# Kernel tuning notes

Measured on AMD Instinct MI355X. Metric: run time of the kernel, lower is better.

## Reference

```python
import jax, jax.numpy as jnp
import numpy as np

D_MODEL = 1024
NUM_HEADS = 16
D_HEAD = D_MODEL // NUM_HEADS
D_FF = 4096
B, T = 2, 2048
THETA = 10000.0
EPS = 1e-5


def setup_inputs() -> dict:
    key = jax.random.key(0)
    ks = jax.random.split(key, 6)
    def tn(k, shape, fan_in, fan_out):
        std = np.sqrt(2.0 / (fan_in + fan_out))
        return jax.random.normal(k, shape, dtype=jnp.float32) * std
    return {
        "x": jax.random.normal(ks[0], (B, T, D_MODEL), dtype=jnp.float32),
        "W_qkv": tn(ks[1], (3 * D_MODEL, D_MODEL), D_MODEL, 3 * D_MODEL),
        "W_o": tn(ks[2], (D_MODEL, D_MODEL), D_MODEL, D_MODEL),
        "g1": jnp.ones((D_MODEL,), dtype=jnp.float32),
        "g2": jnp.ones((D_MODEL,), dtype=jnp.float32),
        "W1": tn(ks[3], (D_FF, D_MODEL), D_MODEL, D_FF),
        "W2": tn(ks[4], (D_MODEL, D_FF), D_FF, D_MODEL),
        "W3": tn(ks[5], (D_FF, D_MODEL), D_MODEL, D_FF),
    }


def _rmsnorm(x, g):
    xf = x.astype(jnp.float32)
    rms = jnp.sqrt(jnp.mean(xf * xf, axis=-1, keepdims=True) + EPS)
    return (xf / rms * g).astype(x.dtype)


def _rope(t, cos, sin):
    # t: [B,H,T,dh]; interleaved (even,odd) pairs treated as complex numbers
    tr = t.reshape(*t.shape[:-1], D_HEAD // 2, 2)
    te, to = tr[..., 0], tr[..., 1]
    out = jnp.stack([te * cos - to * sin, te * sin + to * cos], axis=-1)
    return out.reshape(t.shape)


def reference(x, W_qkv, W_o, g1, g2, W1, W2, W3):
    Bx, Tx, C = x.shape
    # --- attention sub-block (pre-norm) ---
    h = _rmsnorm(x, g1)
    qkv = jnp.einsum('btc,jc->btj', h, W_qkv)                # [B,T,3C]
    qkv = qkv.reshape(Bx, Tx, 3, NUM_HEADS, D_HEAD)
    qkv = jnp.transpose(qkv, (2, 0, 3, 1, 4))                # [3,B,H,T,dh]
    q, k, v = qkv[0], qkv[1], qkv[2]
    # RoPE tables for positions arange(T)
    inv = 1.0 / (THETA ** (jnp.arange(0, D_HEAD, 2, dtype=jnp.float32) / D_HEAD))
    ang = jnp.arange(Tx, dtype=jnp.float32)[:, None] * inv[None, :]   # [T,dh/2]
    cos, sin = jnp.cos(ang), jnp.sin(ang)                    # broadcast over B,H
    q = _rope(q, cos, sin)
    k = _rope(k, cos, sin)
    scores = jnp.einsum('bhqd,bhkd->bhqk', q, k) / jnp.sqrt(jnp.float32(D_HEAD))
    causal = jnp.tril(jnp.ones((Tx, Tx), dtype=bool))
    scores = jnp.where(causal, scores, -jnp.inf)
    probs = jax.nn.softmax(scores, axis=-1)
    attn = jnp.einsum('bhqk,bhkd->bhqd', probs, v)           # [B,H,T,dh]
    attn = jnp.transpose(attn, (0, 2, 1, 3)).reshape(Bx, Tx, C)
    x = x + jnp.einsum('btc,jc->btj', attn, W_o)
    # --- SwiGLU FFN sub-block (pre-norm) ---
    h2 = _rmsnorm(x, g2)
    a = jnp.einsum('btc,fc->btf', h2, W1)
    b = jnp.einsum('btc,fc->btf', h2, W3)
    ffn = jnp.einsum('btf,cf->btc', (a * jax.nn.sigmoid(a)) * b, W2)
    return x + ffn
```

## Files before the change

### kernel.cpp

```cpp
#include <hip/hip_runtime.h>
#include <math.h>

typedef __bf16 bf16_t;
typedef __bf16 bf16x2 __attribute__((ext_vector_type(2)));
typedef __bf16 bf16x4 __attribute__((ext_vector_type(4)));
typedef __bf16 bf16x8 __attribute__((ext_vector_type(8)));
typedef float  f32x4  __attribute__((ext_vector_type(4)));

#define D_MODEL 1024
#define T_SEQ   2048
#define BATCH   2
#define NHEAD   16
#define DHEAD   64
#define DFF     4096
#define ROWS    (BATCH * T_SEQ)

static __device__ __forceinline__ void gload_lds16(const void* g, void* l) {
  __builtin_amdgcn_global_load_lds((const __attribute__((address_space(1))) void*)g,
                                   (__attribute__((address_space(3))) void*)l,
                                   16, 0, 0);
}

__global__ __launch_bounds__(256) void cvt_all_kernel(const float* __restrict__ Wqkv,
                                                      const float* __restrict__ Wo,
                                                      const float* __restrict__ W1,
                                                      const float* __restrict__ W3,
                                                      const float* __restrict__ W2,
                                                      bf16_t* __restrict__ wq,
                                                      bf16_t* __restrict__ wo,
                                                      bf16_t* __restrict__ w13,
                                                      bf16_t* __restrict__ w2) {
  int i = blockIdx.x * 256 + threadIdx.x;
  const float* src; bf16_t* dst; int off;
  if (i < 786432)       { src = Wqkv; dst = wq;            off = i; }
  else if (i < 1048576) { src = Wo;   dst = wo;            off = i - 786432; }
  else if (i < 2097152) { src = W1;   dst = w13;           off = i - 1048576; }
  else if (i < 3145728) { src = W3;   dst = w13 + 4194304; off = i - 2097152; }
  else                  { src = W2;   dst = w2;            off = i - 3145728; }
  float4 v = ((const float4*)src)[off];
  bf16x4 o;
  o[0] = (bf16_t)v.x; o[1] = (bf16_t)v.y; o[2] = (bf16_t)v.z; o[3] = (bf16_t)v.w;
  *(bf16x4*)(dst + off * 4) = o;
}

__global__ __launch_bounds__(256) void rope_tables_kernel(float* __restrict__ cost,
                                                          float* __restrict__ sint) {
  int i = blockIdx.x * 256 + threadIdx.x;
  int t = i >> 5, p = i & 31;
  double inv = pow(10000.0, -(double)(2 * p) / 64.0);
  double ang = (double)t * inv;
  cost[i] = (float)cos(ang);
  sint[i] = (float)sin(ang);
}

__global__ __launch_bounds__(256) void rmsnorm_kernel(const float* __restrict__ x,
                                                      const float* __restrict__ g,
                                                      bf16_t* __restrict__ out) {
  const int row = blockIdx.x;
  const int tid = threadIdx.x;
  const float4 v = ((const float4*)(x + (size_t)row * D_MODEL))[tid];
  float ss = v.x * v.x + v.y * v.y + v.z * v.z + v.w * v.w;
#pragma unroll
  for (int m = 32; m >= 1; m >>= 1) ss += __shfl_xor(ss, m);
  __shared__ float red[4];
  if ((tid & 63) == 0) red[tid >> 6] = ss;
  __syncthreads();
  float tot = red[0] + red[1] + red[2] + red[3];
  const float rinv = 1.0f / sqrtf(tot * (1.0f / D_MODEL) + 1e-5f);
  const float4 gv = ((const float4*)g)[tid];
  bf16x4 o;
  o[0] = (bf16_t)(v.x * rinv * gv.x);
  o[1] = (bf16_t)(v.y * rinv * gv.y);
  o[2] = (bf16_t)(v.z * rinv * gv.z);
  o[3] = (bf16_t)(v.w * rinv * gv.w);
  *(bf16x4*)(out + (size_t)row * D_MODEL + tid * 4) = o;
}

__global__ __launch_bounds__(256) void rope_scatter_kernel(const bf16_t* __restrict__ qkv,
                                                           const float* __restrict__ cost,
                                                           const float* __restrict__ sint,
                                                           bf16_t* __restrict__ Q,
                                                           bf16_t* __restrict__ K) {
  int i = blockIdx.x * 256 + threadIdx.x;
  int p = i & 31;
  int h = (i >> 5) & 15;
  int t = (i >> 9) & 2047;
  int b = i >> 20;
  const bf16_t* base = qkv + (size_t)(b * T_SEQ + t) * (3 * D_MODEL) + h * DHEAD + 2 * p;
  float qe = (float)base[0],            qo = (float)base[1];
  float ke = (float)base[D_MODEL],      ko = (float)base[D_MODEL + 1];
  float c = cost[t * 32 + p], s = sint[t * 32 + p];
  size_t o = ((size_t)(b * NHEAD + h) * T_SEQ + t) * DHEAD + 2 * p;
  bf16x2 qv, kv;
  qv[0] = (bf16_t)(qe * c - qo * s); qv[1] = (bf16_t)(qe * s + qo * c);
  kv[0] = (bf16_t)(ke * c - ko * s); kv[1] = (bf16_t)(ke * s + ko * c);
  *(bf16x2*)(Q + o) = qv;
  *(bf16x2*)(K + o) = kv;
}

__global__ __launch_bounds__(256) void vt_kernel(const bf16_t* __restrict__ qkv,
                                                 bf16_t* __restrict__ Vt) {
  __shared__ bf16_t ld[64 * 72];
  const int tid = threadIdx.x;
  const int tt = blockIdx.x;
  const int bh = blockIdx.y;
  const int b = bh >> 4, h = bh & 15;
#pragma unroll
  for (int it = 0; it < 2; ++it) {
    int idx = it * 256 + tid;
    int r = idx >> 3, cc = (idx & 7) * 8;
    bf16x8 v = *(const bf16x8*)&qkv[(size_t)(b * T_SEQ + tt * 64 + r) * (3 * D_MODEL)
                                    + 2 * D_MODEL + h * DHEAD + cc];
    *(bf16x8*)&ld[r * 72 + cc] = v;
  }
  __syncthreads();
#pragma unroll
  for (int it = 0; it < 2; ++it) {
    int idx = it * 256 + tid;
    int d = idx >> 3, t8 = (idx & 7) * 8;
    bf16x8 v;
#pragma unroll
    for (int j = 0; j < 8; ++j) v[j] = ld[(t8 + j) * 72 + d];
    *(bf16x8*)&Vt[(((size_t)bh * 32 + tt) * 64 + d) * 64 + t8] = v;
  }
}

template <int EPI, int BM, int BN>
__global__ __launch_bounds__(256) void gemm_bt(const bf16_t* __restrict__ A,
                                               const bf16_t* __restrict__ B,
                                               void* __restrict__ Cout,
                                               const float* __restrict__ res,
                                               int M, int N, int K, int lda, int gxn) {
  constexpr int MR = BM / 32, NR = BN / 32;
  __shared__ __align__(16) bf16_t lA[BM * 64];
  __shared__ __align__(16) bf16_t lB[BN * 64];
  const int tid = threadIdx.x;
  const int wave = tid >> 6, lane = tid & 63;
  const int lr = lane & 15, lg = lane >> 4;
  const int nwg = gridDim.x;
  const int bid = blockIdx.x;
  const int swz = (bid & 7) * (nwg >> 3) + (bid >> 3);
  const int bx = swz % gxn, by = swz / gxn;
  const int brow = by * BM, bcol = bx * BN;
  const int wr = (wave >> 1) * (BM / 2), wc = (wave & 1) * (BN / 2);
  f32x4 acc[MR][NR] = {};
  for (int k0 = 0; k0 < K; k0 += 64) {
    __syncthreads();
#pragma unroll
    for (int r = 0; r < BM / 32; ++r) {
      const int base = r * 4096 + wave * 1024;
      const int fb = base + lane * 16;
      const int row = fb >> 7;
      const int e = (fb & 127) >> 1;
      gload_lds16(A + (size_t)(brow + row) * lda + k0 + e, (char*)lA + base);
    }
#pragma unroll
    for (int r = 0; r < BN / 32; ++r) {
      const int base = r * 4096 + wave * 1024;
      const int fb = base + lane * 16;
      const int row = fb >> 7;
      const int e = (fb & 127) >> 1;
      gload_lds16(B + (size_t)(bcol + row) * K + k0 + e, (char*)lB + base);
    }
    __syncthreads();
    bf16x8 aF[MR][2], bF[NR][2];
#pragma unroll
    for (int mi = 0; mi < MR; ++mi)
#pragma unroll
      for (int h = 0; h < 2; ++h)
        aF[mi][h] = *(const bf16x8*)&lA[(wr + mi * 16 + lr) * 64 + h * 32 + 8 * lg];
#pragma unroll
    for (int ni = 0; ni < NR; ++ni)
#pragma unroll
      for (int h = 0; h < 2; ++h)
        bF[ni][h] = *(const bf16x8*)&lB[(wc + ni * 16 + lr) * 64 + h * 32 + 8 * lg];
#pragma unroll
    for (int h = 0; h < 2; ++h)
#pragma unroll
      for (int mi = 0; mi < MR; ++mi)
#pragma unroll
        for (int ni = 0; ni < NR; ++ni)
          acc[mi][ni] = __builtin_amdgcn_mfma_f32_16x16x32_bf16(aF[mi][h], bF[ni][h], acc[mi][ni], 0, 0, 0);
  }
  const int rb = brow + wr + lg * 4;
  const int cb = bcol + wc + lr;
  if (EPI == 0) {
    bf16_t* C = (bf16_t*)Cout;
#pragma unroll
    for (int mi = 0; mi < MR; ++mi)
#pragma unroll
      for (int ni = 0; ni < NR; ++ni)
#pragma unroll
        for (int i = 0; i < 4; ++i)
          C[(size_t)(rb + mi * 16 + i) * N + cb + ni * 16] = (bf16_t)acc[mi][ni][i];
  } else {
    float* C = (float*)Cout;
#pragma unroll
    for (int mi = 0; mi < MR; ++mi)
#pragma unroll
      for (int ni = 0; ni < NR; ++ni)
#pragma unroll
        for (int i = 0; i < 4; ++i) {
          size_t idx = (size_t)(rb + mi * 16 + i) * N + cb + ni * 16;
          C[idx] = acc[mi][ni][i] + res[idx];
        }
  }
}

__global__ __launch_bounds__(256, 4) void attn_kernel(const bf16_t* __restrict__ Q,
                                                      const bf16_t* __restrict__ K,
                                                      const bf16_t* __restrict__ Vt,
                                                      bf16_t* __restrict__ attn) {
  __shared__ __align__(16) bf16_t kbuf[2][64 * 64];
  __shared__ __align__(16) bf16_t vbuf[2][64 * 64];
  __shared__ __align__(16) bf16_t pbuf[4][16 * 64];
  const int tid = threadIdx.x;
  const int wave = tid >> 6, lane = tid & 63;
  const int lr = lane & 15, lg = lane >> 4;
  const int bid = blockIdx.x;
  const int x = bid & 7, u = bid >> 3;
  const int bh = x * 4 + (u & 3);
  const int v = u >> 2;
  const int tile = (7 * v + 5 * (u & 3) + x) & 31;
  const int b = bh >> 4, hh = bh & 15;
  const size_t hb = (size_t)bh * T_SEQ * DHEAD;
  const bf16_t* Qb = Q + hb;
  const bf16_t* Kb = K + hb;
  const bf16_t* Vb = Vt + hb;
  char* pwc = (char*)pbuf[wave];
  const int q0 = tile * 64 + wave * 16;
  const int c0 = wave * 2, c1 = wave * 2 + 1;
  const int so = (lane * 16) ^ ((lane >> 3) << 4);

  bf16x8 qf[2];
#pragma unroll
  for (int h = 0; h < 2; ++h)
    qf[h] = *(const bf16x8*)&Qb[(size_t)(q0 + lr) * DHEAD + h * 32 + 8 * lg];
  f32x4 o[4] = {};
  float mrun = -INFINITY, lsum = 0.0f;
  const int nit = tile + 1;

  {
    const char* kg = (const char*)Kb;
    const char* vg = (const char*)Vb;
    gload_lds16(kg + c0 * 1024 + so, (char*)kbuf[0] + c0 * 1024);
    gload_lds16(kg + c1 * 1024 + so, (char*)kbuf[0] + c1 * 1024);
    gload_lds16(vg + c0 * 1024 + so, (char*)vbuf[0] + c0 * 1024);
    gload_lds16(vg + c1 * 1024 + so, (char*)vbuf[0] + c1 * 1024);
  }
  __syncthreads();
  int cur = 0;

  for (int it = 0; it < nit; ++it) {
    const int k0 = it * 64;
    if (it + 1 < nit) {
      const char* kg = (const char*)(Kb + (size_t)(k0 + 64) * DHEAD);
      const char* vg = (const char*)(Vb + (size_t)(it + 1) * 4096);
      char* kd = (char*)kbuf[cur ^ 1];
      char* vd = (char*)vbuf[cur ^ 1];
      gload_lds16(kg + c0 * 1024 + so, kd + c0 * 1024);
      gload_lds16(kg + c1 * 1024 + so, kd + c1 * 1024);
      gload_lds16(vg + c0 * 1024 + so, vd + c0 * 1024);
      gload_lds16(vg + c1 * 1024 + so, vd + c1 * 1024);
    }
    const char* kl = (const char*)kbuf[cur];
    const char* vl = (const char*)vbuf[cur];
    f32x4 s[4] = {};
#pragma unroll
    for (int c = 0; c < 4; ++c) {
      const int tr = c * 16 + lr;
      const int sw = (tr & 7) << 4;
      bf16x8 kf0 = *(const bf16x8*)(kl + tr * 128 + ((16 * lg) ^ sw));
      bf16x8 kf1 = *(const bf16x8*)(kl + tr * 128 + ((64 + 16 * lg) ^ sw));
      s[c] = __builtin_amdgcn_mfma_f32_16x16x32_bf16(kf0, qf[0], s[c], 0, 0, 0);
      s[c] = __builtin_amdgcn_mfma_f32_16x16x32_bf16(kf1, qf[1], s[c], 0, 0, 0);
    }
    const bool dm = (k0 + 63 > q0);
#pragma unroll
    for (int c = 0; c < 4; ++c)
#pragma unroll
      for (int i = 0; i < 4; ++i) {
        float sv = s[c][i] * 0.125f;
        if (dm && (k0 + c * 16 + lg * 4 + i > q0 + lr)) sv = -INFINITY;
        s[c][i] = sv;
      }
    float bm = s[0][0];
#pragma unroll
    for (int c = 0; c < 4; ++c)
#pragma unroll
      for (int i = 0; i < 4; ++i) bm = fmaxf(bm, s[c][i]);
    bm = fmaxf(bm, __shfl_xor(bm, 16));
    bm = fmaxf(bm, __shfl_xor(bm, 32));
    if (!__all(bm <= mrun)) {
      const float mn = fmaxf(mrun, bm);
      const float al = __expf(mrun - mn);
      mrun = mn;
      lsum *= al;
#pragma unroll
      for (int dd = 0; dd < 4; ++dd)
#pragma unroll
        for (int i = 0; i < 4; ++i) o[dd][i] *= al;
    }
    float bs = 0.0f;
#pragma unroll
    for (int c = 0; c < 4; ++c)
#pragma unroll
      for (int i = 0; i < 4; ++i) {
        float e = __expf(s[c][i] - mrun);
        s[c][i] = e;
        bs += e;
      }
    bs += __shfl_xor(bs, 16);
    bs += __shfl_xor(bs, 32);
    lsum += bs;
#pragma unroll
    for (int c = 0; c < 4; ++c) {
      bf16x4 pb;
#pragma unroll
      for (int i = 0; i < 4; ++i) pb[i] = (bf16_t)s[c][i];
      const int byt = (lr * 128 + ((c * 32 + lg * 8) ^ ((lr & 7) << 4)));
      *(bf16x4*)(pwc + byt) = pb;
    }
    asm volatile("s_waitcnt lgkmcnt(0)" ::: "memory");
    __builtin_amdgcn_sched_barrier(0);
    bf16x8 pT[2];
#pragma unroll
    for (int h = 0; h < 2; ++h)
      pT[h] = *(const bf16x8*)(pwc + (lr * 128 + ((h * 64 + 16 * lg) ^ ((lr & 7) << 4))));
#pragma unroll
    for (int dd = 0; dd < 4; ++dd) {
      const int vr = dd * 16 + lr;
      const int sw = (vr & 7) << 4;
      bf16x8 vf0 = *(const bf16x8*)(vl + vr * 128 + ((16 * lg) ^ sw));
      bf16x8 vf1 = *(const bf16x8*)(vl + vr * 128 + ((64 + 16 * lg) ^ sw));
      o[dd] = __builtin_amdgcn_mfma_f32_16x16x32_bf16(vf0, pT[0], o[dd], 0, 0, 0);
      o[dd] = __builtin_amdgcn_mfma_f32_16x16x32_bf16(vf1, pT[1], o[dd], 0, 0, 0);
    }
    __syncthreads();
    cur ^= 1;
  }
  const float rls = 1.0f / lsum;
  bf16_t* orow = attn + (size_t)(b * T_SEQ + q0 + lr) * D_MODEL + hh * DHEAD;
#pragma unroll
  for (int dd = 0; dd < 4; ++dd) {
    bf16x4 ov;
#pragma unroll
    for (int i = 0; i < 4; ++i) ov[i] = (bf16_t)(o[dd][i] * rls);
    *(bf16x4*)(orow + dd * 16 + lg * 4) = ov;
  }
}

__global__ __launch_bounds__(256) void swiglu_kernel(bf16_t* __restrict__ a13) {
  int i = blockIdx.x * 256 + threadIdx.x;
  int r = i >> 9;
  int c = (i & 511) * 8;
  bf16_t* pa = a13 + (size_t)r * 8192 + c;
  bf16x8 va = *(const bf16x8*)pa;
  bf16x8 vb = *(const bf16x8*)(pa + 4096);
  bf16x8 og;
#pragma unroll
  for (int j = 0; j < 8; ++j) {
    float av = (float)va[j];
    float bv = (float)vb[j];
    float gv = av / (1.0f + __expf(-av)) * bv;
    og[j] = (bf16_t)gv;
  }
  *(bf16x8*)pa = og;
}

extern "C" void kernel_launch(void* const* d_in, const int* in_sizes, int n_in,
                              void* d_out, int out_size, void* d_ws, size_t ws_size,
                              hipStream_t stream) {
  const float* x    = (const float*)d_in[0];
  const float* Wqkv = (const float*)d_in[1];
  const float* Wo   = (const float*)d_in[2];
  const float* g1   = (const float*)d_in[3];
  const float* g2   = (const float*)d_in[4];
  const float* W1   = (const float*)d_in[5];
  const float* W2   = (const float*)d_in[6];
  const float* W3   = (const float*)d_in[7];
  float* out = (float*)d_out;
  char* ws = (char*)d_ws;
  const size_t MB = 1024 * 1024;

  float*  x1    = (float*)(ws + 0);
  bf16_t* h     = (bf16_t*)(ws + 16 * MB);
  bf16_t* attn  = (bf16_t*)(ws + 16 * MB);
  bf16_t* h2    = (bf16_t*)(ws + 16 * MB);
  bf16_t* qkv   = (bf16_t*)(ws + 24 * MB);
  bf16_t* Qb    = (bf16_t*)(ws + 48 * MB);
  bf16_t* Kb    = (bf16_t*)(ws + 56 * MB);
  bf16_t* Vt    = (bf16_t*)(ws + 64 * MB);
  bf16_t* ab13  = (bf16_t*)(ws + 24 * MB);
  bf16_t* wq_b  = (bf16_t*)(ws + 88 * MB);
  bf16_t* wo_b  = (bf16_t*)(ws + 94 * MB);
  bf16_t* w13_b = (bf16_t*)(ws + 96 * MB);
  bf16_t* w2_b  = (bf16_t*)(ws + 112 * MB);
  float*  cost  = (float*)(ws + 120 * MB);
  float*  sint  = (float*)(ws + 120 * MB + 262144);

  cvt_all_kernel<<<16384, 256, 0, stream>>>(Wqkv, Wo, W1, W3, W2, wq_b, wo_b, w13_b, w2_b);
  rope_tables_kernel<<<(T_SEQ * 32) / 256, 256, 0, stream>>>(cost, sint);

  rmsnorm_kernel<<<ROWS, 256, 0, stream>>>(x, g1, h);
  gemm_bt<0, 128, 128><<<768, 256, 0, stream>>>(h, wq_b, qkv, nullptr,
                                                ROWS, 3 * D_MODEL, D_MODEL, D_MODEL, 24);
  rope_scatter_kernel<<<(BATCH * T_SEQ * NHEAD * 32) / 256, 256, 0, stream>>>(
      qkv, cost, sint, Qb, Kb);
  vt_kernel<<<dim3(T_SEQ / 64, BATCH * NHEAD), 256, 0, stream>>>(qkv, Vt);
  attn_kernel<<<1024, 256, 0, stream>>>(Qb, Kb, Vt, attn);
  gemm_bt<1, 128, 64><<<512, 256, 0, stream>>>(attn, wo_b, x1, x,
                                               ROWS, D_MODEL, D_MODEL, D_MODEL, 16);

  rmsnorm_kernel<<<ROWS, 256, 0, stream>>>(x1, g2, h2);
  gemm_bt<0, 128, 128><<<2048, 256, 0, stream>>>(h2, w13_b, ab13, nullptr,
                                                 ROWS, 2 * DFF, D_MODEL, D_MODEL, 64);
  swiglu_kernel<<<(ROWS * DFF) / (256 * 8), 256, 0, stream>>>(ab13);
  gemm_bt<1, 128, 64><<<512, 256, 0, stream>>>(ab13, w2_b, out, x1,
                                               ROWS, D_MODEL, DFF, 2 * DFF, 16);
}
```

Before: 473.7 us.

## Add double-buffered 256x256 GEMM with swizzled LDS for QKV and W13 projections

```diff
diff --git a/kernel.cpp b/kernel.cpp
--- a/kernel.cpp
+++ b/kernel.cpp
@@ -123,6 +123,107 @@
     for (int j = 0; j < 8; ++j) v[j] = ld[(t8 + j) * 72 + d];
     *(bf16x8*)&Vt[(((size_t)bh * 32 + tt) * 64 + d) * 64 + t8] = v;
   }
+}
+
+__global__ __launch_bounds__(512, 2) void gemm256(const bf16_t* __restrict__ A,
+                                                  const bf16_t* __restrict__ B,
+                                                  bf16_t* __restrict__ C,
+                                                  int M, int N, int K, int lda, int gxn) {
+  __shared__ __align__(16) bf16_t lA[2][256 * 64];
+  __shared__ __align__(16) bf16_t lB[2][256 * 64];
+  const int tid = threadIdx.x;
+  const int wave = tid >> 6, lane = tid & 63;
+  const int lr = lane & 15, lg = lane >> 4;
+  const int wm = wave >> 2, wn = wave & 3;
+  const int nwg = gridDim.x;
+  const int bid = blockIdx.x;
+  const int swz = (bid & 7) * (nwg >> 3) + (bid >> 3);
+  const int bx = swz % gxn, by = swz / gxn;
+  const int brow = by * 256, bcol = bx * 256;
+  const bf16_t* __restrict__ Ab = A + (size_t)brow * lda;
+  const bf16_t* __restrict__ Bb = B + (size_t)bcol * K;
+  const int NT = K >> 6;
+
+  auto stage_half = [&](const bf16_t* __restrict__ G, int ld, int k0, char* lbuf, int hh) {
+#pragma unroll
+    for (int r = 0; r < 2; ++r) {
+      const int db = hh * 16384 + r * 8192 + wave * 1024;
+      const int d = db + lane * 16;
+      const int row = d >> 7;
+      const int cb = (d & 127) ^ ((row & 7) << 4);
+      gload_lds16((const char*)(G + (size_t)row * ld + k0) + cb, lbuf + db);
+    }
+  };
+
+  f32x4 acc[8][4] = {};
+
+  stage_half(Ab, lda, 0, (char*)lA[0], 0);
+  stage_half(Ab, lda, 0, (char*)lA[0], 1);
+  stage_half(Bb, K, 0, (char*)lB[0], 0);
+  stage_half(Bb, K, 0, (char*)lB[0], 1);
+  asm volatile("s_waitcnt vmcnt(0)" ::: "memory");
+  __builtin_amdgcn_s_barrier();
+
+  for (int t = 0; t < NT; ++t) {
+    const int p = t & 1;
+    const int k0 = t * 64;
+    const char* pA = (const char*)lA[p];
+    const char* pB = (const char*)lB[p];
+    char* nA = (char*)lA[p ^ 1];
+    char* nB = (char*)lB[p ^ 1];
+#pragma unroll
+    for (int q = 0; q < 4; ++q) {
+      const int qr = q >> 1, qc = q & 1;
+      bf16x8 aF[4][2], bF[2][2];
+#pragma unroll
+      for (int mi = 0; mi < 4; ++mi) {
+        const int ar = wm * 128 + qr * 64 + mi * 16 + lr;
+#pragma unroll
+        for (int h = 0; h < 2; ++h)
+          aF[mi][h] = *(const bf16x8*)(pA + ar * 128 + ((h * 64 + lg * 16) ^ ((ar & 7) << 4)));
+      }
+#pragma unroll
+      for (int ni = 0; ni < 2; ++ni) {
+        const int br_ = wn * 64 + qc * 32 + ni * 16 + lr;
+#pragma unroll
+        for (int h = 0; h < 2; ++h)
+          bF[ni][h] = *(const bf16x8*)(pB + br_ * 128 + ((h * 64 + lg * 16) ^ ((br_ & 7) << 4)));
+      }
+      if (t + 1 < NT) {
+        if (q == 0) {
+          stage_half(Ab, lda, k0 + 64, nA, 0);
+          stage_half(Ab, lda, k0 + 64, nA, 1);
+        } else if (q == 1) {
+          stage_half(Bb, K, k0 + 64, nB, 0);
+          stage_half(Bb, K, k0 + 64, nB, 1);
+        }
+      }
+      __builtin_amdgcn_s_barrier();
+      asm volatile("s_waitcnt lgkmcnt(0)" ::: "memory");
+      __builtin_amdgcn_sched_barrier(0);
+      __builtin_amdgcn_s_setprio(1);
+#pragma unroll
+      for (int h = 0; h < 2; ++h)
+#pragma unroll
+        for (int mi = 0; mi < 4; ++mi)
+#pragma unroll
+          for (int ni = 0; ni < 2; ++ni)
+            acc[qr * 4 + mi][qc * 2 + ni] = __builtin_amdgcn_mfma_f32_16x16x32_bf16(
+                aF[mi][h], bF[ni][h], acc[qr * 4 + mi][qc * 2 + ni], 0, 0, 0);
+      __builtin_amdgcn_s_setprio(0);
+      if (q == 3 && t + 1 < NT)
+        asm volatile("s_waitcnt vmcnt(0)" ::: "memory");
+      __builtin_amdgcn_s_barrier();
+    }
+  }
+#pragma unroll
+  for (int Mi = 0; Mi < 8; ++Mi)
+#pragma unroll
+    for (int Ni = 0; Ni < 4; ++Ni)
+#pragma unroll
+      for (int i = 0; i < 4; ++i)
+        C[(size_t)(brow + wm * 128 + Mi * 16 + lg * 4 + i) * N + bcol + wn * 64 + Ni * 16 + lr] =
+            (bf16_t)acc[Mi][Ni][i];
 }
 
 template <int EPI, int BM, int BN>
@@ -151,29 +252,33 @@
       const int base = r * 4096 + wave * 1024;
       const int fb = base + lane * 16;
       const int row = fb >> 7;
-      const int e = (fb & 127) >> 1;
-      gload_lds16(A + (size_t)(brow + row) * lda + k0 + e, (char*)lA + base);
+      const int cb = (fb & 127) ^ ((row & 7) << 4);
+      gload_lds16((const char*)(A + (size_t)(brow + row) * lda + k0) + cb, (char*)lA + base);
     }
 #pragma unroll
     for (int r = 0; r < BN / 32; ++r) {
       const int base = r * 4096 + wave * 1024;
       const int fb = base + lane * 16;
       const int row = fb >> 7;
-      const int e = (fb & 127) >> 1;
-      gload_lds16(B + (size_t)(bcol + row) * K + k0 + e, (char*)lB + base);
+      const int cb = (fb & 127) ^ ((row & 7) << 4);
+      gload_lds16((const char*)(B + (size_t)(bcol + row) * K + k0) + cb, (char*)lB + base);
     }
     __syncthreads();
     bf16x8 aF[MR][2], bF[NR][2];
 #pragma unroll
-    for (int mi = 0; mi < MR; ++mi)
+    for (int mi = 0; mi < MR; ++mi) {
+      const int ar = wr + mi * 16 + lr;
 #pragma unroll
       for (int h = 0; h < 2; ++h)
-        aF[mi][h] = *(const bf16x8*)&lA[(wr + mi * 16 + lr) * 64 + h * 32 + 8 * lg];
-#pragma unroll
-    for (int ni = 0; ni < NR; ++ni)
+        aF[mi][h] = *(const bf16x8*)((const char*)lA + ar * 128 + ((h * 64 + lg * 16) ^ ((ar & 7) << 4)));
+    }
+#pragma unroll
+    for (int ni = 0; ni < NR; ++ni) {
+      const int br_ = wc + ni * 16 + lr;
 #pragma unroll
       for (int h = 0; h < 2; ++h)
-        bF[ni][h] = *(const bf16x8*)&lB[(wc + ni * 16 + lr) * 64 + h * 32 + 8 * lg];
+        bF[ni][h] = *(const bf16x8*)((const char*)lB + br_ * 128 + ((h * 64 + lg * 16) ^ ((br_ & 7) << 4)));
+    }
 #pragma unroll
     for (int h = 0; h < 2; ++h)
 #pragma unroll
@@ -183,7 +288,7 @@
           acc[mi][ni] = __builtin_amdgcn_mfma_f32_16x16x32_bf16(aF[mi][h], bF[ni][h], acc[mi][ni], 0, 0, 0);
   }
   const int rb = brow + wr + lg * 4;
-  const int cb = bcol + wc + lr;
+  const int cb2 = bcol + wc + lr;
   if (EPI == 0) {
     bf16_t* C = (bf16_t*)Cout;
 #pragma unroll
@@ -192,7 +297,7 @@
       for (int ni = 0; ni < NR; ++ni)
 #pragma unroll
         for (int i = 0; i < 4; ++i)
-          C[(size_t)(rb + mi * 16 + i) * N + cb + ni * 16] = (bf16_t)acc[mi][ni][i];
+          C[(size_t)(rb + mi * 16 + i) * N + cb2 + ni * 16] = (bf16_t)acc[mi][ni][i];
   } else {
     float* C = (float*)Cout;
 #pragma unroll
@@ -201,7 +306,7 @@
       for (int ni = 0; ni < NR; ++ni)
 #pragma unroll
         for (int i = 0; i < 4; ++i) {
-          size_t idx = (size_t)(rb + mi * 16 + i) * N + cb + ni * 16;
+          size_t idx = (size_t)(rb + mi * 16 + i) * N + cb2 + ni * 16;
           C[idx] = acc[mi][ni][i] + res[idx];
         }
   }
@@ -403,8 +508,7 @@
   rope_tables_kernel<<<(T_SEQ * 32) / 256, 256, 0, stream>>>(cost, sint);
 
   rmsnorm_kernel<<<ROWS, 256, 0, stream>>>(x, g1, h);
-  gemm_bt<0, 128, 128><<<768, 256, 0, stream>>>(h, wq_b, qkv, nullptr,
-                                                ROWS, 3 * D_MODEL, D_MODEL, D_MODEL, 24);
+  gemm256<<<192, 512, 0, stream>>>(h, wq_b, qkv, ROWS, 3 * D_MODEL, D_MODEL, D_MODEL, 12);
   rope_scatter_kernel<<<(BATCH * T_SEQ * NHEAD * 32) / 256, 256, 0, stream>>>(
       qkv, cost, sint, Qb, Kb);
   vt_kernel<<<dim3(T_SEQ / 64, BATCH * NHEAD), 256, 0, stream>>>(qkv, Vt);
@@ -413,8 +517,7 @@
                                                ROWS, D_MODEL, D_MODEL, D_MODEL, 16);
 
   rmsnorm_kernel<<<ROWS, 256, 0, stream>>>(x1, g2, h2);
-  gemm_bt<0, 128, 128><<<2048, 256, 0, stream>>>(h2, w13_b, ab13, nullptr,
-                                                 ROWS, 2 * DFF, D_MODEL, D_MODEL, 64);
+  gemm256<<<512, 512, 0, stream>>>(h2, w13_b, ab13, ROWS, 2 * DFF, D_MODEL, D_MODEL, 32);
   swiglu_kernel<<<(ROWS * DFF) / (256 * 8), 256, 0, stream>>>(ab13);
   gemm_bt<1, 128, 64><<<512, 256, 0, stream>>>(ab13, w2_b, out, x1,
                                                ROWS, D_MODEL, DFF, 2 * DFF, 16);
```

Measured after the change: 418.7 us. -11.6%, faster.
